# Kernel optimization log

Measured on AMD Instinct MI355X. Metric: run time of the kernel, lower is better.

The kernel has to match this reference:

```python
import jax, jax.numpy as jnp
import numpy as np
import math

B, L, HID, H = 4, 1024, 1024, 16
DH = HID // H              # 64
MAX_SEQ = 1024             # hard-coded in module


def setup_inputs() -> dict:
    key = jax.random.key(0)
    ks = jax.random.split(key, 6)
    s = 0.02  # small init scale (stands in for xavier)
    return {
        "x": jax.random.normal(ks[0], (B, L, HID), jnp.float32),
        "Wq": jax.random.normal(ks[1], (HID, HID), jnp.float32) * s,
        "bq": jnp.zeros((HID,), jnp.float32),
        "Wk": jax.random.normal(ks[2], (HID, HID), jnp.float32) * s,
        "bk": jnp.zeros((HID,), jnp.float32),
        "Wv": jax.random.normal(ks[3], (HID, HID), jnp.float32) * s,
        "bv": jnp.zeros((HID,), jnp.float32),
        "Wo": jax.random.normal(ks[4], (HID, HID), jnp.float32) * s,
        "bo": jnp.zeros((HID,), jnp.float32),
        "rel_emb": jax.random.normal(ks[5], (2 * MAX_SEQ - 1, DH), jnp.float32) * s,
    }


def reference(x, Wq, bq, Wk, bk, Wv, bv, Wo, bo, rel_emb):
    b, l, hid = x.shape
    dh = rel_emb.shape[1]
    h = hid // dh
    max_seq = (rel_emb.shape[0] + 1) // 2

    def heads(y):
        return y.reshape(b, l, h, dh).transpose(0, 2, 1, 3)  # [B,H,L,dh]

    q = heads(x @ Wq + bq)
    k = heads(x @ Wk + bk)
    v = heads(x @ Wv + bv)

    scores = jnp.einsum("bhid,bhjd->bhij", q, k) / math.sqrt(dh)
    scores = jnp.clip(scores, -100000.0, 100000.0)

    # relative position bias: rel_pos[i,j] = rel_emb[i - j + max_seq - 1]
    pos_idx = jnp.arange(l)[:, None] - jnp.arange(l)[None, :] + max_seq - 1
    rel_pos = rel_emb[pos_idx]                          # [L,L,dh]
    scores = scores + jnp.einsum("bhid,ijd->bhij", q, rel_pos)

    attn = jax.nn.softmax(scores, axis=-1)
    attn = attn / (attn.sum(axis=-1, keepdims=True) + 1e-8)  # faithful renorm
    # dropout is identity in eval mode

    ctx = jnp.einsum("bhij,bhjd->bhid", attn, v)
    ctx = ctx.transpose(0, 2, 1, 3).reshape(b, l, hid)
    return ctx @ Wo + bo
```

## Files before the change

kernel.cpp:

```cpp
#include <hip/hip_runtime.h>
#include <cstddef>

#define B_ 4
#define L_ 1024
#define H_ 16
#define DH_ 64
#define HID_ 1024
#define HEADSZ_ 4194304

typedef short bf16x8 __attribute__((ext_vector_type(8)));
typedef short bf16x4 __attribute__((ext_vector_type(4)));
typedef float f32x4  __attribute__((ext_vector_type(4)));

__device__ __forceinline__ short f2bf(float f) {
    unsigned u = __float_as_uint(f);
    u = (u + 0x7fffu + ((u >> 16) & 1u)) >> 16;
    return (short)u;
}
__device__ __forceinline__ float bf2f(short s) {
    return __uint_as_float(((unsigned)(unsigned short)s) << 16);
}
__device__ __forceinline__ void glds16(const short* g, short* l) {
    __builtin_amdgcn_global_load_lds(
        (const __attribute__((address_space(1))) unsigned int*)g,
        (__attribute__((address_space(3))) unsigned int*)l, 16, 0, 0);
}

__global__ __launch_bounds__(256) void prep_k(
    const float* __restrict__ x,
    const float* __restrict__ Wq, const float* __restrict__ Wk,
    const float* __restrict__ Wv, const float* __restrict__ Wo,
    const float* __restrict__ rel,
    short* __restrict__ xb, short* __restrict__ Wt, short* __restrict__ relimg)
{
    const int bid = blockIdx.x;
    const int t   = threadIdx.x;
    if (bid < 2048) {
        const int base = (bid * 256 + t) << 3;
        float4 f0 = *(const float4*)&x[base];
        float4 f1 = *(const float4*)&x[base + 4];
        bf16x8 p;
        p[0] = f2bf(f0.x); p[1] = f2bf(f0.y); p[2] = f2bf(f0.z); p[3] = f2bf(f0.w);
        p[4] = f2bf(f1.x); p[5] = f2bf(f1.y); p[6] = f2bf(f1.z); p[7] = f2bf(f1.w);
        *(bf16x8*)&xb[base] = p;
    } else if (bid < 3072) {
        const int idx = bid - 2048;
        const int z = idx >> 8, tile = idx & 255;
        const float* W = (z == 0) ? Wq : (z == 1) ? Wk : (z == 2) ? Wv : Wo;
        short* dstb = Wt + (size_t)z * HID_ * HID_;
        __shared__ float T[64][65];
        const int k0 = (tile & 15) << 6, n0 = (tile >> 4) << 6;
        const int r  = t & 63;
        const int cg = t >> 6;
#pragma unroll
        for (int u = 0; u < 4; ++u) {
            float4 f = *(const float4*)&W[(size_t)(k0 + r) * HID_ + n0 + (cg << 4) + (u << 2)];
            T[r][(cg << 4) + (u << 2) + 0] = f.x;
            T[r][(cg << 4) + (u << 2) + 1] = f.y;
            T[r][(cg << 4) + (u << 2) + 2] = f.z;
            T[r][(cg << 4) + (u << 2) + 3] = f.w;
        }
        __syncthreads();
        bf16x8 p0, p1;
#pragma unroll
        for (int j = 0; j < 8; ++j) p0[j] = f2bf(T[(cg << 4) + j][r]);
#pragma unroll
        for (int j = 0; j < 8; ++j) p1[j] = f2bf(T[(cg << 4) + 8 + j][r]);
        short* dst = &dstb[(size_t)(n0 + r) * HID_ + k0 + (cg << 4)];
        *(bf16x8*)dst       = p0;
        *(bf16x8*)(dst + 8) = p1;
    } else {
        const int base = ((bid - 3072) * 256 + t) << 3;
        if (base >= 2047 * 64) return;
        const int r = base >> 6, d0 = base & 63;
        float4 f0 = *(const float4*)&rel[base];
        float4 f1 = *(const float4*)&rel[base + 4];
        bf16x8 p;
        p[0] = f2bf(f0.x); p[1] = f2bf(f0.y); p[2] = f2bf(f0.z); p[3] = f2bf(f0.w);
        p[4] = f2bf(f1.x); p[5] = f2bf(f1.y); p[6] = f2bf(f1.z); p[7] = f2bf(f1.w);
        const size_t dst = ((size_t)(r >> 6) << 12) + ((r & 63) << 6)
                         + ((((d0 >> 3) ^ (r & 7))) << 3);
        *(bf16x8*)&relimg[dst] = p;
    }
}

__global__ __launch_bounds__(256, 2) void gemm_glds_k(
    const short* __restrict__ A, const short* __restrict__ Wt,
    const float* __restrict__ b0, const float* __restrict__ b1,
    const float* __restrict__ b2, void* __restrict__ outv,
    int K, int mode)
{
    __shared__ short As[128 * 64];
    __shared__ short Bs[128 * 64];

    const int t    = threadIdx.x;
    const int lane = t & 63, w = t >> 6;
    const int m0   = blockIdx.y << 7, n0 = blockIdx.x << 7;
    const int fr   = lane & 15, qd = lane >> 4;
    const int wm0  = (w & 1) << 6, wn0 = (w >> 1) << 6;

    const int lr = lane >> 3;
    const int sg = (lane & 7) ^ lr;

    f32x4 acc[4][4];
#pragma unroll
    for (int i = 0; i < 4; ++i)
#pragma unroll
        for (int j = 0; j < 4; ++j) acc[i][j] = (f32x4){0.f, 0.f, 0.f, 0.f};

    const short* aBase = A  + (size_t)(m0 + w * 32 + lr) * K + sg * 8;
    const short* bBase = Wt + (size_t)(n0 + w * 32 + lr) * K + sg * 8;
    short* aDst = &As[(w * 32) * 64];
    short* bDst = &Bs[(w * 32) * 64];

    for (int k0 = 0; k0 < K; k0 += 64) {
        __syncthreads();
#pragma unroll
        for (int g = 0; g < 4; ++g) {
            glds16(aBase + (size_t)(g * 8) * K + k0, aDst + g * 8 * 64);
            glds16(bBase + (size_t)(g * 8) * K + k0, bDst + g * 8 * 64);
        }
        __syncthreads();

#pragma unroll
        for (int hh2 = 0; hh2 < 2; ++hh2) {
            const int kg = (hh2 << 2) + qd;
            bf16x8 af[4], bfv[4];
#pragma unroll
            for (int mt = 0; mt < 4; ++mt) {
                const int row = wm0 + (mt << 4) + fr;
                af[mt] = *(const bf16x8*)&As[(row << 6) + ((kg ^ (row & 7)) << 3)];
            }
#pragma unroll
            for (int nt = 0; nt < 4; ++nt) {
                const int row = wn0 + (nt << 4) + fr;
                bfv[nt] = *(const bf16x8*)&Bs[(row << 6) + ((kg ^ (row & 7)) << 3)];
            }
#pragma unroll
            for (int mt = 0; mt < 4; ++mt)
#pragma unroll
                for (int nt = 0; nt < 4; ++nt)
                    acc[mt][nt] = __builtin_amdgcn_mfma_f32_16x16x32_bf16(
                        af[mt], bfv[nt], acc[mt][nt], 0, 0, 0);
        }
    }

#pragma unroll
    for (int nt = 0; nt < 4; ++nt) {
        const int coln = n0 + wn0 + (nt << 4) + fr;
        float bias;
        if (mode == 0) bias = b0[coln];
        else {
            const int t3 = coln >> 10;
            bias = (t3 == 0 ? b0 : t3 == 1 ? b1 : b2)[coln & 1023];
        }
#pragma unroll
        for (int mt = 0; mt < 4; ++mt)
#pragma unroll
            for (int rg = 0; rg < 4; ++rg) {
                const int row = m0 + wm0 + (mt << 4) + (qd << 2) + rg;
                const float val = acc[mt][nt][rg] + bias;
                if (mode == 0) {
                    ((float*)outv)[(size_t)row * HID_ + coln] = val;
                } else {
                    const int t3 = coln >> 10;
                    const int h  = (coln >> 6) & 15;
                    const int d  = coln & 63;
                    const int bb = row >> 10, l = row & 1023;
                    const size_t bhoff = ((size_t)(bb * H_ + h)) << 16;
                    size_t dst;
                    if (t3 == 0)
                        dst = bhoff + ((size_t)l << 6) + d;
                    else if (t3 == 1)
                        dst = (size_t)HEADSZ_ + bhoff + ((size_t)(l >> 6) << 12)
                            + ((l & 63) << 6) + ((((d >> 3) ^ (l & 7))) << 3) + (d & 7);
                    else
                        dst = 2 * (size_t)HEADSZ_ + bhoff + ((size_t)(l >> 6) << 12)
                            + ((size_t)d << 6) + (((((l >> 3) & 7) ^ (d & 7))) << 3) + (l & 7);
                    ((short*)outv)[dst] = f2bf(val);
                }
            }
    }
}

__global__ __launch_bounds__(256, 3) void attn_mfma_k(
    const short* __restrict__ q, const short* __restrict__ kimg,
    const short* __restrict__ vimg, const short* __restrict__ relimg,
    short* __restrict__ ctx)
{
    __shared__ __align__(16) short Ks[64 * 64];
    __shared__ __align__(16) short Vt[64 * 64];
    __shared__ __align__(16) short Rl[64 * 64];
    __shared__ __align__(16) short Ts[2 * 64 * 68];
    __shared__ __align__(16) short Ps[64 * 72];

    const int t    = threadIdx.x;
    const int i0   = blockIdx.x << 6;
    const int h    = blockIdx.y;
    const int b    = blockIdx.z;
    const size_t bh = (size_t)(b * H_ + h) << 16;
    const int lane = t & 63, w = t >> 6;
    const int fr   = lane & 15, qd = lane >> 4;
    const int m16  = i0 >> 6;
    const int iiB  = (w << 4) + (qd << 2);
    const int soff = w * 1024 + lane * 8;

    bf16x8 af[2];
#pragma unroll
    for (int hh = 0; hh < 2; ++hh)
        af[hh] = *(const bf16x8*)&q[bh + ((size_t)(i0 + (w << 4) + fr) << 6)
                                    + (((hh << 2) + qd) << 3)];

    glds16(relimg + ((size_t)(m16 + 16) << 12) + soff,       Rl + w * 1024);
    glds16(relimg + ((size_t)(m16 + 16) << 12) + soff + 512, Rl + w * 1024 + 512);
    __syncthreads();
    {
        f32x4 acc_t[4];
#pragma unroll
        for (int i = 0; i < 4; ++i) acc_t[i] = (f32x4){0.f, 0.f, 0.f, 0.f};
#pragma unroll
        for (int hh = 0; hh < 2; ++hh) {
            const int g = (hh << 2) + qd;
#pragma unroll
            for (int rt = 0; rt < 4; ++rt) {
                const int rr = (rt << 4) + fr;
                bf16x8 br = *(const bf16x8*)&Rl[(rr << 6) + ((g ^ (rr & 7)) << 3)];
                acc_t[rt] = __builtin_amdgcn_mfma_f32_16x16x32_bf16(af[hh], br, acc_t[rt], 0, 0, 0);
            }
        }
        const int pu = m16 & 1;
#pragma unroll
        for (int rt = 0; rt < 4; ++rt) {
            bf16x4 p;
            p[0] = f2bf(acc_t[rt][0]); p[1] = f2bf(acc_t[rt][1]);
            p[2] = f2bf(acc_t[rt][2]); p[3] = f2bf(acc_t[rt][3]);
            *(bf16x4*)&Ts[pu * 4352 + ((rt << 4) + fr) * 68 + iiB] = p;
        }
    }

    f32x4 acc_o[4];
#pragma unroll
    for (int i = 0; i < 4; ++i) acc_o[i] = (f32x4){0.f, 0.f, 0.f, 0.f};
    float den[4] = {0.f, 0.f, 0.f, 0.f};

    for (int jt = 0; jt < 16; ++jt) {
        const int mlow = m16 + 15 - jt;
        const int pl   = mlow & 1;

        __syncthreads();
        glds16(kimg + bh + ((size_t)jt << 12) + soff,       Ks + w * 1024);
        glds16(kimg + bh + ((size_t)jt << 12) + soff + 512, Ks + w * 1024 + 512);
        glds16(vimg + bh + ((size_t)jt << 12) + soff,       Vt + w * 1024);
        glds16(vimg + bh + ((size_t)jt << 12) + soff + 512, Vt + w * 1024 + 512);
        glds16(relimg + ((size_t)mlow << 12) + soff,        Rl + w * 1024);
        glds16(relimg + ((size_t)mlow << 12) + soff + 512,  Rl + w * 1024 + 512);
        __syncthreads();

        f32x4 acc_s[4];
#pragma unroll
        for (int i = 0; i < 4; ++i) acc_s[i] = (f32x4){0.f, 0.f, 0.f, 0.f};
#pragma unroll
        for (int hh = 0; hh < 2; ++hh) {
            const int g = (hh << 2) + qd;
#pragma unroll
            for (int nt = 0; nt < 4; ++nt) {
                const int rb = (nt << 4) + fr;
                bf16x8 bk = *(const bf16x8*)&Ks[(rb << 6) + ((g ^ (rb & 7)) << 3)];
                acc_s[nt] = __builtin_amdgcn_mfma_f32_16x16x32_bf16(af[hh], bk, acc_s[nt], 0, 0, 0);
            }
        }

        {
            f32x4 acc_t[4];
#pragma unroll
            for (int i = 0; i < 4; ++i) acc_t[i] = (f32x4){0.f, 0.f, 0.f, 0.f};
#pragma unroll
            for (int hh = 0; hh < 2; ++hh) {
                const int g = (hh << 2) + qd;
#pragma unroll
                for (int rt = 0; rt < 4; ++rt) {
                    const int rr = (rt << 4) + fr;
                    bf16x8 br = *(const bf16x8*)&Rl[(rr << 6) + ((g ^ (rr & 7)) << 3)];
                    acc_t[rt] = __builtin_amdgcn_mfma_f32_16x16x32_bf16(af[hh], br, acc_t[rt], 0, 0, 0);
                }
            }
#pragma unroll
            for (int rt = 0; rt < 4; ++rt) {
                bf16x4 p;
                p[0] = f2bf(acc_t[rt][0]); p[1] = f2bf(acc_t[rt][1]);
                p[2] = f2bf(acc_t[rt][2]); p[3] = f2bf(acc_t[rt][3]);
                *(bf16x4*)&Ts[pl * 4352 + ((rt << 4) + fr) * 68 + iiB] = p;
            }
        }

#pragma unroll
        for (int nt = 0; nt < 4; ++nt) {
            const int jj = (nt << 4) + fr;
#pragma unroll
            for (int rg = 0; rg < 4; ++rg) {
                const int ii = iiB + rg;
                const int r7 = ii - jj + 63;
                const int par = pl ^ (r7 >> 6);
                const float tv = bf2f(Ts[par * 4352 + (r7 & 63) * 68 + ii]);
                float s = acc_s[nt][rg] * 0.125f;
                s = fminf(fmaxf(s, -100000.f), 100000.f);
                const float e = __expf(s + tv);
                den[rg] += e;
                Ps[ii * 72 + jj] = f2bf(e);
            }
        }

#pragma unroll
        for (int hh = 0; hh < 2; ++hh) {
            const int g = (hh << 2) + qd;
            bf16x8 ap = *(const bf16x8*)&Ps[((w << 4) + fr) * 72 + (g << 3)];
#pragma unroll
            for (int nt = 0; nt < 4; ++nt) {
                const int rb = (nt << 4) + fr;
                bf16x8 bv = *(const bf16x8*)&Vt[(rb << 6) + ((g ^ (rb & 7)) << 3)];
                acc_o[nt] = __builtin_amdgcn_mfma_f32_16x16x32_bf16(ap, bv, acc_o[nt], 0, 0, 0);
            }
        }
    }

#pragma unroll
    for (int off = 1; off < 16; off <<= 1)
#pragma unroll
        for (int rg = 0; rg < 4; ++rg)
            den[rg] += __shfl_xor(den[rg], off);

#pragma unroll
    for (int rg = 0; rg < 4; ++rg) {
        const float inv = 1.0f / den[rg];
        const int l = i0 + iiB + rg;
#pragma unroll
        for (int nt = 0; nt < 4; ++nt)
            ctx[((size_t)(b * L_ + l) << 10) + (h << 6) + (nt << 4) + fr] =
                f2bf(acc_o[nt][rg] * inv);
    }
}

extern "C" void kernel_launch(void* const* d_in, const int* in_sizes, int n_in,
                              void* d_out, int out_size, void* d_ws, size_t ws_size,
                              hipStream_t stream)
{
    const float* x   = (const float*)d_in[0];
    const float* Wq  = (const float*)d_in[1];
    const float* bq  = (const float*)d_in[2];
    const float* Wk  = (const float*)d_in[3];
    const float* bk  = (const float*)d_in[4];
    const float* Wv  = (const float*)d_in[5];
    const float* bv  = (const float*)d_in[6];
    const float* Wo  = (const float*)d_in[7];
    const float* bo  = (const float*)d_in[8];
    const float* rel = (const float*)d_in[9];
    float* out = (float*)d_out;

    short* xb     = (short*)d_ws;
    short* qkv    = xb + (size_t)HEADSZ_;
    short* cw     = qkv + (size_t)3 * HEADSZ_;
    short* wt     = cw + (size_t)HEADSZ_;
    short* relimg = wt + (size_t)4 * HID_ * HID_;

    const dim3 tb(256);

    prep_k<<<dim3(3136), tb, 0, stream>>>(x, Wq, Wk, Wv, Wo, rel, xb, wt, relimg);

    gemm_glds_k<<<dim3(24, 32), tb, 0, stream>>>(
        xb, wt, bq, bk, bv, qkv, HID_, 1);

    attn_mfma_k<<<dim3(16, H_, B_), tb, 0, stream>>>(
        qkv, qkv + HEADSZ_, qkv + 2 * (size_t)HEADSZ_, relimg, cw);

    gemm_glds_k<<<dim3(8, 32), tb, 0, stream>>>(
        cw, wt + (size_t)3 * HID_ * HID_, bo, bo, bo, out, HID_, 0);
}
```

Measured before the change: 225.4 us.

## Double-buffer attention K/V/rel tiles and shrink GEMM k-tile for higher occupancy

The attention kernel now double-buffers the K, V and relative-embedding tiles in LDS. It prefetches tile jt+1 while computing tile jt and drops the second barrier per iteration. This doubles that LDS footprint, so its occupancy hint falls from 3 to 2. Separately, the projection GEMM halves its k-tile to 32 with a new swizzle and raises its occupancy hint to 3, trading twice as many barrier-separated k-steps for more resident waves. The attention overlap depends on the compiler not inserting full memory waits before the LDS reads.

Measured after the change: 234.3 us. +4.0%, slower.

```diff
diff --git a/kernel.cpp b/kernel.cpp
--- a/kernel.cpp
+++ b/kernel.cpp
@@ -84,14 +84,14 @@
     }
 }
 
-__global__ __launch_bounds__(256, 2) void gemm_glds_k(
+__global__ __launch_bounds__(256, 3) void gemm_glds_k(
     const short* __restrict__ A, const short* __restrict__ Wt,
     const float* __restrict__ b0, const float* __restrict__ b1,
     const float* __restrict__ b2, void* __restrict__ outv,
     int K, int mode)
 {
-    __shared__ short As[128 * 64];
-    __shared__ short Bs[128 * 64];
+    __shared__ short As[128 * 32];
+    __shared__ short Bs[128 * 32];
 
     const int t    = threadIdx.x;
     const int lane = t & 63, w = t >> 6;
@@ -99,8 +99,9 @@
     const int fr   = lane & 15, qd = lane >> 4;
     const int wm0  = (w & 1) << 6, wn0 = (w >> 1) << 6;
 
-    const int lr = lane >> 3;
-    const int sg = (lane & 7) ^ lr;
+    const int srow = lane >> 2;
+    const int sg   = (lane & 3) ^ ((lane >> 3) & 3);
+    const int slot = qd ^ ((fr >> 1) & 3);
 
     f32x4 acc[4][4];
 #pragma unroll
@@ -108,41 +109,36 @@
 #pragma unroll
         for (int j = 0; j < 4; ++j) acc[i][j] = (f32x4){0.f, 0.f, 0.f, 0.f};
 
-    const short* aBase = A  + (size_t)(m0 + w * 32 + lr) * K + sg * 8;
-    const short* bBase = Wt + (size_t)(n0 + w * 32 + lr) * K + sg * 8;
-    short* aDst = &As[(w * 32) * 64];
-    short* bDst = &Bs[(w * 32) * 64];
-
-    for (int k0 = 0; k0 < K; k0 += 64) {
+    const short* aBase  = A  + (size_t)(m0 + w * 32 + srow) * K + sg * 8;
+    const short* aBase2 = aBase + (size_t)16 * K;
+    const short* bBase  = Wt + (size_t)(n0 + w * 32 + srow) * K + sg * 8;
+    const short* bBase2 = bBase + (size_t)16 * K;
+    short* aDst  = &As[(w * 32) * 32];
+    short* aDst2 = &As[(w * 32 + 16) * 32];
+    short* bDst  = &Bs[(w * 32) * 32];
+    short* bDst2 = &Bs[(w * 32 + 16) * 32];
+
+    for (int k0 = 0; k0 < K; k0 += 32) {
         __syncthreads();
-#pragma unroll
-        for (int g = 0; g < 4; ++g) {
-            glds16(aBase + (size_t)(g * 8) * K + k0, aDst + g * 8 * 64);
-            glds16(bBase + (size_t)(g * 8) * K + k0, bDst + g * 8 * 64);
-        }
+        glds16(aBase + k0, aDst);
+        glds16(aBase2 + k0, aDst2);
+        glds16(bBase + k0, bDst);
+        glds16(bBase2 + k0, bDst2);
         __syncthreads();
 
-#pragma unroll
-        for (int hh2 = 0; hh2 < 2; ++hh2) {
-            const int kg = (hh2 << 2) + qd;
-            bf16x8 af[4], bfv[4];
-#pragma unroll
-            for (int mt = 0; mt < 4; ++mt) {
-                const int row = wm0 + (mt << 4) + fr;
-                af[mt] = *(const bf16x8*)&As[(row << 6) + ((kg ^ (row & 7)) << 3)];
-            }
-#pragma unroll
-            for (int nt = 0; nt < 4; ++nt) {
-                const int row = wn0 + (nt << 4) + fr;
-                bfv[nt] = *(const bf16x8*)&Bs[(row << 6) + ((kg ^ (row & 7)) << 3)];
-            }
-#pragma unroll
-            for (int mt = 0; mt < 4; ++mt)
-#pragma unroll
-                for (int nt = 0; nt < 4; ++nt)
-                    acc[mt][nt] = __builtin_amdgcn_mfma_f32_16x16x32_bf16(
-                        af[mt], bfv[nt], acc[mt][nt], 0, 0, 0);
-        }
+        bf16x8 af[4], bfv[4];
+#pragma unroll
+        for (int mt = 0; mt < 4; ++mt)
+            af[mt] = *(const bf16x8*)&As[((wm0 + (mt << 4) + fr) << 5) + (slot << 3)];
+#pragma unroll
+        for (int nt = 0; nt < 4; ++nt)
+            bfv[nt] = *(const bf16x8*)&Bs[((wn0 + (nt << 4) + fr) << 5) + (slot << 3)];
+#pragma unroll
+        for (int mt = 0; mt < 4; ++mt)
+#pragma unroll
+            for (int nt = 0; nt < 4; ++nt)
+                acc[mt][nt] = __builtin_amdgcn_mfma_f32_16x16x32_bf16(
+                    af[mt], bfv[nt], acc[mt][nt], 0, 0, 0);
     }
 
 #pragma unroll
@@ -183,14 +179,14 @@
     }
 }
 
-__global__ __launch_bounds__(256, 3) void attn_mfma_k(
+__global__ __launch_bounds__(256, 2) void attn_mfma_k(
     const short* __restrict__ q, const short* __restrict__ kimg,
     const short* __restrict__ vimg, const short* __restrict__ relimg,
     short* __restrict__ ctx)
 {
-    __shared__ __align__(16) short Ks[64 * 64];
-    __shared__ __align__(16) short Vt[64 * 64];
-    __shared__ __align__(16) short Rl[64 * 64];
+    __shared__ __align__(16) short Ks[2][64 * 64];
+    __shared__ __align__(16) short Vt[2][64 * 64];
+    __shared__ __align__(16) short Rl[2][64 * 64];
     __shared__ __align__(16) short Ts[2 * 64 * 68];
     __shared__ __align__(16) short Ps[64 * 72];
 
@@ -211,8 +207,8 @@
         af[hh] = *(const bf16x8*)&q[bh + ((size_t)(i0 + (w << 4) + fr) << 6)
                                     + (((hh << 2) + qd) << 3)];
 
-    glds16(relimg + ((size_t)(m16 + 16) << 12) + soff,       Rl + w * 1024);
-    glds16(relimg + ((size_t)(m16 + 16) << 12) + soff + 512, Rl + w * 1024 + 512);
+    glds16(relimg + ((size_t)(m16 + 16) << 12) + soff,       &Rl[1][w * 1024]);
+    glds16(relimg + ((size_t)(m16 + 16) << 12) + soff + 512, &Rl[1][w * 1024 + 512]);
     __syncthreads();
     {
         f32x4 acc_t[4];
@@ -224,7 +220,7 @@
 #pragma unroll
             for (int rt = 0; rt < 4; ++rt) {
                 const int rr = (rt << 4) + fr;
-                bf16x8 br = *(const bf16x8*)&Rl[(rr << 6) + ((g ^ (rr & 7)) << 3)];
+                bf16x8 br = *(const bf16x8*)&Rl[1][(rr << 6) + ((g ^ (rr & 7)) << 3)];
                 acc_t[rt] = __builtin_amdgcn_mfma_f32_16x16x32_bf16(af[hh], br, acc_t[rt], 0, 0, 0);
             }
         }
@@ -238,23 +234,33 @@
         }
     }
 
+    glds16(kimg + bh + soff,        &Ks[0][w * 1024]);
+    glds16(kimg + bh + soff + 512,  &Ks[0][w * 1024 + 512]);
+    glds16(vimg + bh + soff,        &Vt[0][w * 1024]);
+    glds16(vimg + bh + soff + 512,  &Vt[0][w * 1024 + 512]);
+    glds16(relimg + ((size_t)(m16 + 15) << 12) + soff,       &Rl[0][w * 1024]);
+    glds16(relimg + ((size_t)(m16 + 15) << 12) + soff + 512, &Rl[0][w * 1024 + 512]);
+
     f32x4 acc_o[4];
 #pragma unroll
     for (int i = 0; i < 4; ++i) acc_o[i] = (f32x4){0.f, 0.f, 0.f, 0.f};
     float den[4] = {0.f, 0.f, 0.f, 0.f};
 
     for (int jt = 0; jt < 16; ++jt) {
+        const int cur  = jt & 1, nxt = cur ^ 1;
         const int mlow = m16 + 15 - jt;
         const int pl   = mlow & 1;
 
         __syncthreads();
-        glds16(kimg + bh + ((size_t)jt << 12) + soff,       Ks + w * 1024);
-        glds16(kimg + bh + ((size_t)jt << 12) + soff + 512, Ks + w * 1024 + 512);
-        glds16(vimg + bh + ((size_t)jt << 12) + soff,       Vt + w * 1024);
-        glds16(vimg + bh + ((size_t)jt << 12) + soff + 512, Vt + w * 1024 + 512);
-        glds16(relimg + ((size_t)mlow << 12) + soff,        Rl + w * 1024);
-        glds16(relimg + ((size_t)mlow << 12) + soff + 512,  Rl + w * 1024 + 512);
-        __syncthreads();
+
+        if (jt < 15) {
+            glds16(kimg + bh + ((size_t)(jt + 1) << 12) + soff,       &Ks[nxt][w * 1024]);
+            glds16(kimg + bh + ((size_t)(jt + 1) << 12) + soff + 512, &Ks[nxt][w * 1024 + 512]);
+            glds16(vimg + bh + ((size_t)(jt + 1) << 12) + soff,       &Vt[nxt][w * 1024]);
+            glds16(vimg + bh + ((size_t)(jt + 1) << 12) + soff + 512, &Vt[nxt][w * 1024 + 512]);
+            glds16(relimg + ((size_t)(mlow - 1) << 12) + soff,        &Rl[nxt][w * 1024]);
+            glds16(relimg + ((size_t)(mlow - 1) << 12) + soff + 512,  &Rl[nxt][w * 1024 + 512]);
+        }
 
         f32x4 acc_s[4];
 #pragma unroll
@@ -265,7 +271,7 @@
 #pragma unroll
             for (int nt = 0; nt < 4; ++nt) {
                 const int rb = (nt << 4) + fr;
-                bf16x8 bk = *(const bf16x8*)&Ks[(rb << 6) + ((g ^ (rb & 7)) << 3)];
+                bf16x8 bk = *(const bf16x8*)&Ks[cur][(rb << 6) + ((g ^ (rb & 7)) << 3)];
                 acc_s[nt] = __builtin_amdgcn_mfma_f32_16x16x32_bf16(af[hh], bk, acc_s[nt], 0, 0, 0);
             }
         }
@@ -280,7 +286,7 @@
 #pragma unroll
                 for (int rt = 0; rt < 4; ++rt) {
                     const int rr = (rt << 4) + fr;
-                    bf16x8 br = *(const bf16x8*)&Rl[(rr << 6) + ((g ^ (rr & 7)) << 3)];
+                    bf16x8 br = *(const bf16x8*)&Rl[cur][(rr << 6) + ((g ^ (rr & 7)) << 3)];
                     acc_t[rt] = __builtin_amdgcn_mfma_f32_16x16x32_bf16(af[hh], br, acc_t[rt], 0, 0, 0);
                 }
             }
@@ -317,7 +323,7 @@
 #pragma unroll
             for (int nt = 0; nt < 4; ++nt) {
                 const int rb = (nt << 4) + fr;
-                bf16x8 bv = *(const bf16x8*)&Vt[(rb << 6) + ((g ^ (rb & 7)) << 3)];
+                bf16x8 bv = *(const bf16x8*)&Vt[cur][(rb << 6) + ((g ^ (rb & 7)) << 3)];
                 acc_o[nt] = __builtin_amdgcn_mfma_f32_16x16x32_bf16(ap, bv, acc_o[nt], 0, 0, 0);
             }
         }
```

## Shrink GEMM K-tile, templatize N-tile, and transpose attention MFMA operands

Applied to the files above, without the earlier changes.

The GEMM kernel now uses a 32-wide K step with a new swizzle, is templated on N tiles per wave, and allows 3 blocks per SM. The output projection uses a 128x64 tile with twice as many blocks, to fill more CUs. In attention, the score and PV MFMAs swap operands so each lane holds one query row. That allows packed bf16x4 stores to Ps and ctx and a cheaper row-sum reduction with two shuffles. The smaller K step doubles the number of sync barriers per GEMM.

Result: faster. 218.8 us (-2.9%).

```diff
diff --git a/kernel.cpp b/kernel.cpp
--- a/kernel.cpp
+++ b/kernel.cpp
@@ -84,69 +84,67 @@
     }
 }
 
-__global__ __launch_bounds__(256, 2) void gemm_glds_k(
+template <int NT>
+__global__ __launch_bounds__(256, 3) void gemm_glds_k(
     const short* __restrict__ A, const short* __restrict__ Wt,
     const float* __restrict__ b0, const float* __restrict__ b1,
     const float* __restrict__ b2, void* __restrict__ outv,
     int K, int mode)
 {
-    __shared__ short As[128 * 64];
-    __shared__ short Bs[128 * 64];
+    constexpr int BN = NT * 32;
+    __shared__ short As[128 * 32];
+    __shared__ short Bs[BN * 32];
 
     const int t    = threadIdx.x;
     const int lane = t & 63, w = t >> 6;
-    const int m0   = blockIdx.y << 7, n0 = blockIdx.x << 7;
+    const int m0   = blockIdx.y << 7, n0 = blockIdx.x * BN;
     const int fr   = lane & 15, qd = lane >> 4;
-    const int wm0  = (w & 1) << 6, wn0 = (w >> 1) << 6;
-
-    const int lr = lane >> 3;
-    const int sg = (lane & 7) ^ lr;
-
-    f32x4 acc[4][4];
+    const int wm0  = (w & 1) << 6, wn0 = (w >> 1) * (NT << 4);
+
+    const int srow = lane >> 2;
+    const int sg   = (lane & 3) ^ ((lane >> 3) & 3);
+    const int slot = qd ^ ((fr >> 1) & 3);
+
+    f32x4 acc[4][NT];
 #pragma unroll
     for (int i = 0; i < 4; ++i)
 #pragma unroll
-        for (int j = 0; j < 4; ++j) acc[i][j] = (f32x4){0.f, 0.f, 0.f, 0.f};
-
-    const short* aBase = A  + (size_t)(m0 + w * 32 + lr) * K + sg * 8;
-    const short* bBase = Wt + (size_t)(n0 + w * 32 + lr) * K + sg * 8;
-    short* aDst = &As[(w * 32) * 64];
-    short* bDst = &Bs[(w * 32) * 64];
-
-    for (int k0 = 0; k0 < K; k0 += 64) {
-        __syncthreads();
-#pragma unroll
-        for (int g = 0; g < 4; ++g) {
-            glds16(aBase + (size_t)(g * 8) * K + k0, aDst + g * 8 * 64);
-            glds16(bBase + (size_t)(g * 8) * K + k0, bDst + g * 8 * 64);
-        }
-        __syncthreads();
-
-#pragma unroll
-        for (int hh2 = 0; hh2 < 2; ++hh2) {
-            const int kg = (hh2 << 2) + qd;
-            bf16x8 af[4], bfv[4];
-#pragma unroll
-            for (int mt = 0; mt < 4; ++mt) {
-                const int row = wm0 + (mt << 4) + fr;
-                af[mt] = *(const bf16x8*)&As[(row << 6) + ((kg ^ (row & 7)) << 3)];
-            }
-#pragma unroll
-            for (int nt = 0; nt < 4; ++nt) {
-                const int row = wn0 + (nt << 4) + fr;
-                bfv[nt] = *(const bf16x8*)&Bs[(row << 6) + ((kg ^ (row & 7)) << 3)];
-            }
-#pragma unroll
-            for (int mt = 0; mt < 4; ++mt)
-#pragma unroll
-                for (int nt = 0; nt < 4; ++nt)
-                    acc[mt][nt] = __builtin_amdgcn_mfma_f32_16x16x32_bf16(
-                        af[mt], bfv[nt], acc[mt][nt], 0, 0, 0);
-        }
-    }
-
-#pragma unroll
-    for (int nt = 0; nt < 4; ++nt) {
+        for (int j = 0; j < NT; ++j) acc[i][j] = (f32x4){0.f, 0.f, 0.f, 0.f};
+
+    const short* aBase  = A  + (size_t)(m0 + w * 32 + srow) * K + sg * 8;
+    const short* aBase2 = aBase + (size_t)16 * K;
+    const short* bBase  = Wt + (size_t)(n0 + w * (BN / 4) + srow) * K + sg * 8;
+    const short* bBase2 = bBase + (size_t)16 * K;
+    short* aDst  = &As[(w * 32) * 32];
+    short* aDst2 = &As[(w * 32 + 16) * 32];
+    short* bDst  = &Bs[(w * (BN / 4)) * 32];
+    short* bDst2 = &Bs[(w * (BN / 4) + 16) * 32];
+
+    for (int k0 = 0; k0 < K; k0 += 32) {
+        __syncthreads();
+        glds16(aBase + k0, aDst);
+        glds16(aBase2 + k0, aDst2);
+        glds16(bBase + k0, bDst);
+        if (NT == 4) glds16(bBase2 + k0, bDst2);
+        __syncthreads();
+
+        bf16x8 af[4], bfv[NT];
+#pragma unroll
+        for (int mt = 0; mt < 4; ++mt)
+            af[mt] = *(const bf16x8*)&As[((wm0 + (mt << 4) + fr) << 5) + (slot << 3)];
+#pragma unroll
+        for (int nt = 0; nt < NT; ++nt)
+            bfv[nt] = *(const bf16x8*)&Bs[((wn0 + (nt << 4) + fr) << 5) + (slot << 3)];
+#pragma unroll
+        for (int mt = 0; mt < 4; ++mt)
+#pragma unroll
+            for (int nt = 0; nt < NT; ++nt)
+                acc[mt][nt] = __builtin_amdgcn_mfma_f32_16x16x32_bf16(
+                    af[mt], bfv[nt], acc[mt][nt], 0, 0, 0);
+    }
+
+#pragma unroll
+    for (int nt = 0; nt < NT; ++nt) {
         const int coln = n0 + wn0 + (nt << 4) + fr;
         float bias;
         if (mode == 0) bias = b0[coln];
@@ -203,6 +201,7 @@
     const int fr   = lane & 15, qd = lane >> 4;
     const int m16  = i0 >> 6;
     const int iiB  = (w << 4) + (qd << 2);
+    const int ii   = (w << 4) + fr;
     const int soff = w * 1024 + lane * 8;
 
     bf16x8 af[2];
@@ -241,7 +240,7 @@
     f32x4 acc_o[4];
 #pragma unroll
     for (int i = 0; i < 4; ++i) acc_o[i] = (f32x4){0.f, 0.f, 0.f, 0.f};
-    float den[4] = {0.f, 0.f, 0.f, 0.f};
+    float den = 0.f;
 
     for (int jt = 0; jt < 16; ++jt) {
         const int mlow = m16 + 15 - jt;
@@ -263,10 +262,10 @@
         for (int hh = 0; hh < 2; ++hh) {
             const int g = (hh << 2) + qd;
 #pragma unroll
-            for (int nt = 0; nt < 4; ++nt) {
-                const int rb = (nt << 4) + fr;
+            for (int mt = 0; mt < 4; ++mt) {
+                const int rb = (mt << 4) + fr;
                 bf16x8 bk = *(const bf16x8*)&Ks[(rb << 6) + ((g ^ (rb & 7)) << 3)];
-                acc_s[nt] = __builtin_amdgcn_mfma_f32_16x16x32_bf16(af[hh], bk, acc_s[nt], 0, 0, 0);
+                acc_s[mt] = __builtin_amdgcn_mfma_f32_16x16x32_bf16(bk, af[hh], acc_s[mt], 0, 0, 0);
             }
         }
 
@@ -294,49 +293,47 @@
         }
 
 #pragma unroll
-        for (int nt = 0; nt < 4; ++nt) {
-            const int jj = (nt << 4) + fr;
+        for (int mt = 0; mt < 4; ++mt) {
+            bf16x4 pk;
 #pragma unroll
             for (int rg = 0; rg < 4; ++rg) {
-                const int ii = iiB + rg;
-                const int r7 = ii - jj + 63;
-                const int par = pl ^ (r7 >> 6);
-                const float tv = bf2f(Ts[par * 4352 + (r7 & 63) * 68 + ii]);
-                float s = acc_s[nt][rg] * 0.125f;
+                const int jj = (mt << 4) + (qd << 2) + rg;
+                const int c  = ii - jj + 63;
+                const int par = pl ^ (c >> 6);
+                const float tv = bf2f(Ts[par * 4352 + (c & 63) * 68 + ii]);
+                float s = acc_s[mt][rg] * 0.125f;
                 s = fminf(fmaxf(s, -100000.f), 100000.f);
                 const float e = __expf(s + tv);
-                den[rg] += e;
-                Ps[ii * 72 + jj] = f2bf(e);
-            }
+                den += e;
+                pk[rg] = f2bf(e);
+            }
+            *(bf16x4*)&Ps[ii * 72 + (mt << 4) + (qd << 2)] = pk;
         }
 
 #pragma unroll
         for (int hh = 0; hh < 2; ++hh) {
             const int g = (hh << 2) + qd;
-            bf16x8 ap = *(const bf16x8*)&Ps[((w << 4) + fr) * 72 + (g << 3)];
-#pragma unroll
-            for (int nt = 0; nt < 4; ++nt) {
-                const int rb = (nt << 4) + fr;
-                bf16x8 bv = *(const bf16x8*)&Vt[(rb << 6) + ((g ^ (rb & 7)) << 3)];
-                acc_o[nt] = __builtin_amdgcn_mfma_f32_16x16x32_bf16(ap, bv, acc_o[nt], 0, 0, 0);
-            }
-        }
-    }
-
-#pragma unroll
-    for (int off = 1; off < 16; off <<= 1)
-#pragma unroll
-        for (int rg = 0; rg < 4; ++rg)
-            den[rg] += __shfl_xor(den[rg], off);
-
-#pragma unroll
-    for (int rg = 0; rg < 4; ++rg) {
-        const float inv = 1.0f / den[rg];
-        const int l = i0 + iiB + rg;
-#pragma unroll
-        for (int nt = 0; nt < 4; ++nt)
-            ctx[((size_t)(b * L_ + l) << 10) + (h << 6) + (nt << 4) + fr] =
-                f2bf(acc_o[nt][rg] * inv);
+            bf16x8 bp = *(const bf16x8*)&Ps[ii * 72 + (g << 3)];
+#pragma unroll
+            for (int mt = 0; mt < 4; ++mt) {
+                const int rb = (mt << 4) + fr;
+                bf16x8 av = *(const bf16x8*)&Vt[(rb << 6) + ((g ^ (rb & 7)) << 3)];
+                acc_o[mt] = __builtin_amdgcn_mfma_f32_16x16x32_bf16(av, bp, acc_o[mt], 0, 0, 0);
+            }
+        }
+    }
+
+    den += __shfl_xor(den, 16);
+    den += __shfl_xor(den, 32);
+    const float inv = 1.0f / den;
+
+    const int l = i0 + ii;
+#pragma unroll
+    for (int mt = 0; mt < 4; ++mt) {
+        bf16x4 o;
+#pragma unroll
+        for (int rg = 0; rg < 4; ++rg) o[rg] = f2bf(acc_o[mt][rg] * inv);
+        *(bf16x4*)&ctx[((size_t)(b * L_ + l) << 10) + (h << 6) + (mt << 4) + (qd << 2)] = o;
     }
 }
 
@@ -366,12 +363,12 @@
 
     prep_k<<<dim3(3136), tb, 0, stream>>>(x, Wq, Wk, Wv, Wo, rel, xb, wt, relimg);
 
-    gemm_glds_k<<<dim3(24, 32), tb, 0, stream>>>(
+    gemm_glds_k<4><<<dim3(24, 32), tb, 0, stream>>>(
         xb, wt, bq, bk, bv, qkv, HID_, 1);
 
     attn_mfma_k<<<dim3(16, H_, B_), tb, 0, stream>>>(
         qkv, qkv + HEADSZ_, qkv + 2 * (size_t)HEADSZ_, relimg, cw);
 
-    gemm_glds_k<<<dim3(8, 32), tb, 0, stream>>>(
+    gemm_glds_k<2><<<dim3(16, 32), tb, 0, stream>>>(
         cw, wt + (size_t)3 * HID_ * HID_, bo, bo, bo, out, HID_, 0);
 }
```
